# Kernel tuning notes

Hardware: AMD Instinct MI355X
Metric: run time of the kernel (lower is better)

## Reference

```python
import jax, jax.numpy as jnp
import numpy as np

IN_DIM = 128
OUT_DIM = 256
N_ETYPES = 4
N_STEPS = 8
B = 128
N_NODES = 256
E = 393216
CONCAT = IN_DIM + OUT_DIM


def _conv1d(x, w, b):
    # x: [B, C, L], w: [O, I, K] -> valid conv, stride 1
    y = jax.lax.conv_general_dilated(x, w, (1,), 'VALID', dimension_numbers=('NCH', 'OIH', 'NCH'))
    return y + b[None, :, None]


def _maxpool1d(x, k, s):
    return jax.lax.reduce_window(x, -jnp.inf, jax.lax.max, (1, 1, k), (1, 1, s), 'VALID')


def setup_inputs():
    key = jax.random.key(0)
    ks = jax.random.split(key, 16)
    Nn = B * N_NODES
    sc = 0.05
    f32 = jnp.float32
    return {
        'features': jax.random.normal(ks[0], (Nn, IN_DIM), f32),
        'src': jax.random.randint(ks[1], (E,), 0, Nn),
        'dst': jax.random.randint(ks[2], (E,), 0, Nn),
        'etype': jax.random.randint(ks[3], (E,), 0, N_ETYPES),
        'W_msg': jax.random.normal(ks[4], (N_ETYPES, OUT_DIM, OUT_DIM), f32) * sc,
        'b_msg': jnp.zeros((N_ETYPES, OUT_DIM), f32),
        'gru_Wi': jax.random.normal(ks[5], (OUT_DIM, 3 * OUT_DIM), f32) * sc,
        'gru_Wh': jax.random.normal(ks[6], (OUT_DIM, 3 * OUT_DIM), f32) * sc,
        'gru_bi': jnp.zeros((3 * OUT_DIM,), f32),
        'gru_bh': jnp.zeros((3 * OUT_DIM,), f32),
        'conv1_w': jax.random.normal(ks[7], (OUT_DIM, OUT_DIM, 3), f32) * sc,
        'conv1_b': jnp.zeros((OUT_DIM,), f32),
        'conv2_w': jax.random.normal(ks[8], (OUT_DIM, OUT_DIM, 1), f32) * sc,
        'conv2_b': jnp.zeros((OUT_DIM,), f32),
        'convc1_w': jax.random.normal(ks[9], (CONCAT, CONCAT, 3), f32) * sc,
        'convc1_b': jnp.zeros((CONCAT,), f32),
        'convc2_w': jax.random.normal(ks[10], (CONCAT, CONCAT, 1), f32) * sc,
        'convc2_b': jnp.zeros((CONCAT,), f32),
        'wy': jax.random.normal(ks[11], (OUT_DIM, 1), f32) * sc,
        'by': jnp.zeros((1,), f32),
        'wz': jax.random.normal(ks[12], (CONCAT, 1), f32) * sc,
        'bz': jnp.zeros((1,), f32),
        'num_graphs': B,
    }


def reference(features, src, dst, etype, W_msg, b_msg, gru_Wi, gru_Wh, gru_bi, gru_bh,
              conv1_w, conv1_b, conv2_w, conv2_b, convc1_w, convc1_b, convc2_w, convc2_b,
              wy, by, wz, bz, num_graphs):
    Nn = features.shape[0]
    # DGL GatedGraphConv: pad input feats up to out_feats
    h = jnp.pad(features, ((0, 0), (0, OUT_DIM - IN_DIM)))
    for _ in range(N_STEPS):
        # per-etype linear transform of all nodes: [Nn, T, O]
        H_all = jnp.einsum('nd,tdo->nto', h, W_msg) + b_msg[None]
        msg = H_all[src, etype]                              # [E, O]
        a = jax.ops.segment_sum(msg, dst, num_segments=Nn)   # [Nn, O]
        gi = a @ gru_Wi + gru_bi
        gh = h @ gru_Wh + gru_bh
        ir, iz, ig = jnp.split(gi, 3, axis=-1)
        hr, hz, hg = jnp.split(gh, 3, axis=-1)
        r = jax.nn.sigmoid(ir + hr)
        z = jax.nn.sigmoid(iz + hz)
        g = jnp.tanh(ig + r * hg)
        h = (1.0 - z) * g + z * h
    x_i = features.reshape(num_graphs, -1, IN_DIM)
    h_i = h.reshape(num_graphs, -1, OUT_DIM)
    c_i = jnp.concatenate([h_i, x_i], axis=-1)
    Y1 = _maxpool1d(jax.nn.relu(_conv1d(h_i.transpose(0, 2, 1), conv1_w, conv1_b)), 3, 2)
    Y2 = _maxpool1d(jax.nn.relu(_conv1d(Y1, conv2_w, conv2_b)), 2, 2).transpose(0, 2, 1)
    Z1 = _maxpool1d(jax.nn.relu(_conv1d(c_i.transpose(0, 2, 1), convc1_w, convc1_b)), 3, 2)
    Z2 = _maxpool1d(jax.nn.relu(_conv1d(Z1, convc2_w, convc2_b)), 2, 2).transpose(0, 2, 1)
    before_avg = (Y2 @ wy + by) * (Z2 @ wz + bz)   # [B, L, 1]
    avg = before_avg.mean(axis=1)                    # [B, 1]
    return jax.nn.sigmoid(avg).squeeze(-1)           # [B]
```

## Files before the change

### kernel.cpp

```cpp
#include <hip/hip_runtime.h>

#define DEV static __device__ __forceinline__

typedef float f32x4 __attribute__((ext_vector_type(4)));
typedef __bf16 bf16x8 __attribute__((ext_vector_type(8)));
typedef unsigned int u32x4 __attribute__((ext_vector_type(4)));
typedef unsigned int u32x2 __attribute__((ext_vector_type(2)));

#define NNODE 32768
#define NEDGE 393216

DEV unsigned short f2bf(float f) {
    unsigned int u = __builtin_bit_cast(unsigned int, f);
    u += 0x7FFFu + ((u >> 16) & 1u);
    return (unsigned short)(u >> 16);
}
DEV float bf2f(unsigned int b) {
    unsigned int u = b << 16;
    return __builtin_bit_cast(float, u);
}
DEV unsigned int pk2(float a, float b) {
    return (unsigned int)f2bf(a) | ((unsigned int)f2bf(b) << 16);
}
DEV float sigf(float x) { return 1.f / (1.f + __expf(-x)); }

DEV void gld16(const void* g, void* l) {
    __builtin_amdgcn_global_load_lds(
        (const __attribute__((address_space(1))) void*)(g),
        (__attribute__((address_space(3))) void*)(l),
        16, 0, 0);
}


__global__ __launch_bounds__(256) void init_k(
    const float* __restrict__ feat,
    unsigned short* __restrict__ hb0, unsigned short* __restrict__ hb1,
    unsigned short* __restrict__ fb)
{
    int idx = blockIdx.x * 256 + threadIdx.x;
    int r = idx >> 8, c = idx & 255;
    float f = 0.f;
    if (r < NNODE && c < 128) f = feat[(size_t)r * 128 + c];
    unsigned short v = f2bf(f);
    hb0[(size_t)r * 256 + c] = v;
    hb1[(size_t)r * 256 + c] = v;
    if (c < 128) fb[(size_t)r * 128 + c] = v;
}

__global__ __launch_bounds__(256) void prep_wmsg_k(
    const float* __restrict__ Wm, unsigned short* __restrict__ WT)
{
    int idx = blockIdx.x * 256 + threadIdx.x;
    int j = idx >> 8, d = idx & 255;
    int t = j >> 8, o = j & 255;
    WT[idx] = f2bf(Wm[t * 65536 + d * 256 + o]);
}

__global__ __launch_bounds__(256) void prep_gru_k(
    const float* __restrict__ Wi, const float* __restrict__ Wh,
    unsigned short* __restrict__ B2T)
{
    int idx = blockIdx.x * 256 + threadIdx.x;
    int j = idx >> 9, k = idx & 511;
    int band = j >> 6, g = (j >> 4) & 3, ch = (band << 4) + (j & 15);
    float v = 0.f;
    if (g == 0) v = (k < 256) ? Wi[k * 768 + ch] : Wh[(k - 256) * 768 + ch];
    else if (g == 1) v = (k < 256) ? Wi[k * 768 + 256 + ch] : Wh[(k - 256) * 768 + 256 + ch];
    else if (g == 2) { if (k < 256) v = Wi[k * 768 + 512 + ch]; }
    else { if (k >= 256) v = Wh[(k - 256) * 768 + 512 + ch]; }
    B2T[idx] = f2bf(v);
}

__global__ __launch_bounds__(256) void prep_bias2_k(
    const float* __restrict__ bi, const float* __restrict__ bh,
    float* __restrict__ b2)
{
    int j = blockIdx.x * 256 + threadIdx.x;
    int band = j >> 6, g = (j >> 4) & 3, ch = (band << 4) + (j & 15);
    float v;
    if (g == 0) v = bi[ch] + bh[ch];
    else if (g == 1) v = bi[256 + ch] + bh[256 + ch];
    else if (g == 2) v = bi[512 + ch];
    else v = bh[512 + ch];
    b2[j] = v;
}

__global__ __launch_bounds__(256) void prep_conv_k(
    const float* __restrict__ c1w, const float* __restrict__ c2w,
    const float* __restrict__ cc1w, const float* __restrict__ cc2w,
    unsigned short* __restrict__ BTY, unsigned short* __restrict__ BT2,
    unsigned short* __restrict__ BTZ, unsigned short* __restrict__ BTc2)
{
    int idx = blockIdx.x * 256 + threadIdx.x;
    if (idx < 196608) {
        int o = idx / 768, kk = idx - o * 768, k = kk >> 8, c = kk & 255;
        BTY[idx] = f2bf(c1w[o * 768 + c * 3 + k]);
    } else if (idx < 262144) {
        int r = idx - 196608, o = r >> 8, c = r & 255;
        BT2[r] = f2bf(c2w[o * 256 + c]);
    } else if (idx < 704512) {
        int jx = idx - 262144, o = jx / 1152, kk = jx - o * 1152;
        float v;
        if (kk < 768) { int k = kk >> 8, c = kk & 255; v = cc1w[o * 1152 + c * 3 + k]; }
        else { int r = kk - 768, kf = r >> 7, cf = r & 127; v = cc1w[o * 1152 + (256 + cf) * 3 + kf]; }
        BTZ[jx] = f2bf(v);
    } else {
        int r = idx - 704512, o = r / 384, c = r - o * 384;
        BTc2[r] = f2bf(cc2w[o * 384 + c]);
    }
}


__global__ __launch_bounds__(256) void count_k(
    const int* __restrict__ dst, int* __restrict__ cnt)
{
    int e = blockIdx.x * 256 + threadIdx.x;
    atomicAdd(&cnt[dst[e]], 1);
}

__global__ __launch_bounds__(1024) void scan1_k(
    const int* __restrict__ cnt, int* __restrict__ rp, int* __restrict__ bsum)
{
    __shared__ int buf[1024];
    int b = blockIdx.x, tid = threadIdx.x;
    int n = (b << 10) + tid;
    int v = cnt[n];
    buf[tid] = v;
    __syncthreads();
    for (int off = 1; off < 1024; off <<= 1) {
        int x = (tid >= off) ? buf[tid - off] : 0;
        __syncthreads();
        buf[tid] += x;
        __syncthreads();
    }
    rp[n] = buf[tid] - v;
    if (tid == 1023) bsum[b] = buf[1023];
}

__global__ __launch_bounds__(64) void scan2_k(
    const int* __restrict__ bsum, int* __restrict__ boff, int* __restrict__ rp)
{
    int lane = threadIdx.x;
    int v = (lane < 32) ? bsum[lane] : 0;
    int s = v;
    #pragma unroll
    for (int off = 1; off < 32; off <<= 1) {
        int x = __shfl_up(s, off, 64);
        if (lane >= off) s += x;
    }
    if (lane < 32) boff[lane] = s - v;
    if (lane == 31) rp[NNODE] = s;
}

__global__ __launch_bounds__(1024) void scan3_k(
    int* __restrict__ rp, const int* __restrict__ boff)
{
    int b = blockIdx.x, tid = threadIdx.x;
    rp[(b << 10) + tid] += boff[b];
}

__global__ __launch_bounds__(256) void fill_k(
    const int* __restrict__ src, const int* __restrict__ dst,
    const int* __restrict__ et, const int* __restrict__ rp,
    int* __restrict__ pos, int* __restrict__ edat)
{
    int e = blockIdx.x * 256 + threadIdx.x;
    int d = dst[e];
    int p = atomicAdd(&pos[d], 1);
    edat[rp[d] + p] = src[e] | (et[e] << 20);
}


__global__ __launch_bounds__(256) void agg2_k(
    const int* __restrict__ rp, const int* __restrict__ edat,
    const unsigned short* __restrict__ Hmsg, unsigned short* __restrict__ Aonly)
{
    int wave = threadIdx.x >> 6, lane = threadIdx.x & 63;
    int n = (blockIdx.x << 2) + wave;
    int e0 = rp[n], e1 = rp[n + 1];
    float a0 = 0.f, a1 = 0.f, a2 = 0.f, a3 = 0.f;
    const unsigned short* hc = Hmsg + (lane << 2);
    int e = e0;
    for (; e + 8 <= e1; e += 8) {
        u32x2 v[8];
        #pragma unroll
        for (int q = 0; q < 8; q++) {
            int d = edat[e + q];
            v[q] = *(const u32x2*)(hc + ((size_t)(d & 0xFFFFF) << 10) + ((d >> 20) << 8));
        }
        #pragma unroll
        for (int q = 0; q < 8; q++) {
            a0 += bf2f(v[q].x & 0xFFFFu); a1 += bf2f(v[q].x >> 16);
            a2 += bf2f(v[q].y & 0xFFFFu); a3 += bf2f(v[q].y >> 16);
        }
    }
    for (; e < e1; e++) {
        int d = edat[e];
        u32x2 v = *(const u32x2*)(hc + ((size_t)(d & 0xFFFFF) << 10) + ((d >> 20) << 8));
        a0 += bf2f(v.x & 0xFFFFu); a1 += bf2f(v.x >> 16);
        a2 += bf2f(v.y & 0xFFFFu); a3 += bf2f(v.y >> 16);
    }
    u32x2 p; p.x = pk2(a0, a1); p.y = pk2(a2, a3);
    *(u32x2*)(Aonly + (size_t)n * 256 + (lane << 2)) = p;
}

#define STAGE_COORDS                                            \
    int srow[4], scb[4], soff[4];                               \
    _Pragma("unroll")                                           \
    for (int p = 0; p < 4; p++) {                               \
        int c = wave + p * 4;                                   \
        int half = c >> 3, cc = c & 7;                          \
        srow[p] = cc * 16 + (lane >> 2);                        \
        scb[p] = (((lane & 3) ^ ((lane >> 3) & 3)) + half * 4) * 8; \
        soff[p] = half * 4096 + cc * 512;                       \
    }

#define MFMA64(AS, BS)                                                        \
    _Pragma("unroll")                                                         \
    for (int h = 0; h < 2; h++) {                                             \
        bf16x8 af[4], bfr[4];                                                 \
        _Pragma("unroll")                                                     \
        for (int i = 0; i < 4; i++)                                           \
            af[i] = *(const bf16x8*)(&(AS)[h * 4096 + (qm + i * 16 + fm) * 32 + fksw * 8]); \
        _Pragma("unroll")                                                     \
        for (int i = 0; i < 4; i++)                                           \
            bfr[i] = *(const bf16x8*)(&(BS)[h * 4096 + (qn + i * 16 + fm) * 32 + fksw * 8]); \
        _Pragma("unroll")                                                     \
        for (int i = 0; i < 4; i++)                                           \
            _Pragma("unroll")                                                 \
            for (int j = 0; j < 4; j++)                                       \
                acc[i][j] = __builtin_amdgcn_mfma_f32_16x16x32_bf16(bfr[j], af[i], acc[i][j], 0, 0, 0); \
    }

__global__ __launch_bounds__(256) void gemm_bt(
    const unsigned short* __restrict__ A, int lda,
    const unsigned short* __restrict__ Bt,
    unsigned short* __restrict__ Cb, int ldcb,
    const float* __restrict__ bias,
    int N, int K, int swz, int relu)
{
    __shared__ __align__(16) unsigned short As0[128 * 64];
    __shared__ __align__(16) unsigned short As1[128 * 64];
    __shared__ __align__(16) unsigned short Bs0[128 * 64];
    __shared__ __align__(16) unsigned short Bs1[128 * 64];
    const int tid = threadIdx.x;
    int id = blockIdx.x;
    if (swz) { int per = gridDim.x >> 3; id = (id & 7) * per + (id >> 3); }
    const int nb = N >> 7;
    const int bm = id / nb, bn = id - bm * nb;
    const int wave = tid >> 6, lane = tid & 63;
    const unsigned short* Ag = A + (size_t)(bm * 128) * lda;
    const unsigned short* Bg = Bt + (size_t)(bn * 128) * K;
    const int qm = (wave & 1) << 6, qn = (wave >> 1) << 6;
    const int fm = lane & 15, fkv = lane >> 4;
    const int fksw = fkv ^ ((fm >> 1) & 3);
    STAGE_COORDS

    auto stageA = [&](int kb, unsigned short* dst) {
        #pragma unroll
        for (int p = 0; p < 4; p++)
            gld16(Ag + (size_t)srow[p] * lda + kb + scb[p], dst + soff[p]);
    };
    auto stageB = [&](int kb, unsigned short* dst) {
        #pragma unroll
        for (int p = 0; p < 4; p++)
            gld16(Bg + (size_t)srow[p] * K + kb + scb[p], dst + soff[p]);
    };

    f32x4 acc[4][4] = {};

    stageA(0, As0); stageB(0, Bs0);
    __syncthreads();
    unsigned short *Ac = As0, *An = As1, *Bc = Bs0, *Bn = Bs1;
    for (int kb = 0; kb < K; kb += 64) {
        if (kb + 64 < K) { stageA(kb + 64, An); stageB(kb + 64, Bn); }
        MFMA64(Ac, Bc)
        __syncthreads();
        { auto t = Ac; Ac = An; An = t; }
        { auto t = Bc; Bc = Bn; Bn = t; }
    }

    const int m0 = bm * 128 + qm + fm;
    const int n0 = bn * 128 + qn + (fkv << 2);
    #pragma unroll
    for (int i = 0; i < 4; i++) {
        int row = m0 + i * 16;
        #pragma unroll
        for (int j = 0; j < 4; j++) {
            int col = n0 + j * 16;
            float v0 = acc[i][j][0], v1 = acc[i][j][1],
                  v2 = acc[i][j][2], v3 = acc[i][j][3];
            if (bias) {
                float4 bv = *(const float4*)(bias + col);
                v0 += bv.x; v1 += bv.y; v2 += bv.z; v3 += bv.w;
            }
            if (relu) {
                v0 = fmaxf(v0, 0.f); v1 = fmaxf(v1, 0.f);
                v2 = fmaxf(v2, 0.f); v3 = fmaxf(v3, 0.f);
            }
            u32x2 p; p.x = pk2(v0, v1); p.y = pk2(v2, v3);
            *(u32x2*)(Cb + (size_t)row * ldcb + col) = p;
        }
    }
}

__global__ __launch_bounds__(256) void gemm_conv(
    const unsigned short* __restrict__ Ah,
    const unsigned short* __restrict__ Af,
    const unsigned short* __restrict__ Bt,
    unsigned short* __restrict__ Cb, int ldcb,
    const float* __restrict__ bias,
    int N, int K)
{
    __shared__ __align__(16) unsigned short As0[128 * 64];
    __shared__ __align__(16) unsigned short As1[128 * 64];
    __shared__ __align__(16) unsigned short Bs0[128 * 64];
    __shared__ __align__(16) unsigned short Bs1[128 * 64];
    const int tid = threadIdx.x;
    int id = blockIdx.x;
    { int per = gridDim.x >> 3; id = (id & 7) * per + (id >> 3); }
    const int nb = N >> 7;
    const int bm = id / nb, bn = id - bm * nb;
    const int wave = tid >> 6, lane = tid & 63;
    const unsigned short* Bg = Bt + (size_t)(bn * 128) * K;
    const int qm = (wave & 1) << 6, qn = (wave >> 1) << 6;
    const int fm = lane & 15, fkv = lane >> 4;
    const int fksw = fkv ^ ((fm >> 1) & 3);
    STAGE_COORDS

    auto stageA = [&](int kb, unsigned short* dst) {
        const unsigned short* base; int ldA, col, shift;
        if (kb < 768) { base = Ah; ldA = 256; shift = kb >> 8; col = kb & 255; }
        else { int r = kb - 768; base = Af; ldA = 128; shift = r >> 7; col = r & 127; }
        const unsigned short* Ag = base + (size_t)(bm * 128 + shift) * ldA + col;
        #pragma unroll
        for (int p = 0; p < 4; p++)
            gld16(Ag + (size_t)srow[p] * ldA + scb[p], dst + soff[p]);
    };
    auto stageB = [&](int kb, unsigned short* dst) {
        #pragma unroll
        for (int p = 0; p < 4; p++)
            gld16(Bg + (size_t)srow[p] * K + kb + scb[p], dst + soff[p]);
    };

    f32x4 acc[4][4] = {};

    stageA(0, As0); stageB(0, Bs0);
    __syncthreads();
    unsigned short *Ac = As0, *An = As1, *Bc = Bs0, *Bn = Bs1;
    for (int kb = 0; kb < K; kb += 64) {
        if (kb + 64 < K) { stageA(kb + 64, An); stageB(kb + 64, Bn); }
        MFMA64(Ac, Bc)
        __syncthreads();
        { auto t = Ac; Ac = An; An = t; }
        { auto t = Bc; Bc = Bn; Bn = t; }
    }

    const int m0 = bm * 128 + qm + fm;
    const int n0 = bn * 128 + qn + (fkv << 2);
    #pragma unroll
    for (int i = 0; i < 4; i++) {
        int row = m0 + i * 16;
        #pragma unroll
        for (int j = 0; j < 4; j++) {
            int col = n0 + j * 16;
            float4 bv = *(const float4*)(bias + col);
            float v0 = fmaxf(acc[i][j][0] + bv.x, 0.f);
            float v1 = fmaxf(acc[i][j][1] + bv.y, 0.f);
            float v2 = fmaxf(acc[i][j][2] + bv.z, 0.f);
            float v3 = fmaxf(acc[i][j][3] + bv.w, 0.f);
            u32x2 p; p.x = pk2(v0, v1); p.y = pk2(v2, v3);
            *(u32x2*)(Cb + (size_t)row * ldcb + col) = p;
        }
    }
}

__global__ __launch_bounds__(256) void gemm_gru(
    const unsigned short* __restrict__ Aonly,
    const unsigned short* __restrict__ hbc,
    const unsigned short* __restrict__ Bt,
    const float* __restrict__ b2p,
    unsigned short* __restrict__ hbn)
{
    __shared__ __align__(16) unsigned short As0[128 * 64];
    __shared__ __align__(16) unsigned short As1[128 * 64];
    __shared__ __align__(16) unsigned short Bs0[128 * 64];
    __shared__ __align__(16) unsigned short Bs1[128 * 64];
    const int tid = threadIdx.x;
    int id = blockIdx.x;
    { int per = gridDim.x >> 3; id = (id & 7) * per + (id >> 3); }
    const int bm = id >> 3;
    const int bn = id & 7;
    const int wave = tid >> 6, lane = tid & 63;
    const unsigned short* Bg = Bt + (size_t)(bn * 128) * 512;
    const int qm = (wave & 1) << 6, qn = (wave >> 1) << 6;
    const int fm = lane & 15, fkv = lane >> 4;
    const int fksw = fkv ^ ((fm >> 1) & 3);
    STAGE_COORDS

    auto stageA = [&](int kb, unsigned short* dst) {
        const unsigned short* base = (kb < 256) ? Aonly : hbc;
        const unsigned short* Ag = base + (size_t)(bm * 128) * 256 + (kb & 255);
        #pragma unroll
        for (int p = 0; p < 4; p++)
            gld16(Ag + (size_t)srow[p] * 256 + scb[p], dst + soff[p]);
    };
    auto stageB = [&](int kb, unsigned short* dst) {
        #pragma unroll
        for (int p = 0; p < 4; p++)
            gld16(Bg + (size_t)srow[p] * 512 + kb + scb[p], dst + soff[p]);
    };

    f32x4 acc[4][4] = {};

    stageA(0, As0); stageB(0, Bs0);
    __syncthreads();
    unsigned short *Ac = As0, *An = As1, *Bc = Bs0, *Bn = Bs1;
    #pragma unroll
    for (int kb = 0; kb < 512; kb += 64) {
        if (kb < 448) { stageA(kb + 64, An); stageB(kb + 64, Bn); }
        MFMA64(Ac, Bc)
        __syncthreads();
        { auto t = Ac; Ac = An; An = t; }
        { auto t = Bc; Bc = Bn; Bn = t; }
    }

    const int band = (bn << 1) + (qn >> 6);
    const int chb = (band << 4) + (fkv << 2);
    const float4 brv = *(const float4*)(b2p + (band << 6) + 0  + (fkv << 2));
    const float4 bzv = *(const float4*)(b2p + (band << 6) + 16 + (fkv << 2));
    const float4 bgv = *(const float4*)(b2p + (band << 6) + 32 + (fkv << 2));
    const float4 bhv = *(const float4*)(b2p + (band << 6) + 48 + (fkv << 2));
    const float br_[4] = {brv.x, brv.y, brv.z, brv.w};
    const float bz_[4] = {bzv.x, bzv.y, bzv.z, bzv.w};
    const float bg_[4] = {bgv.x, bgv.y, bgv.z, bgv.w};
    const float bh_[4] = {bhv.x, bhv.y, bhv.z, bhv.w};
    const int m0 = bm * 128 + qm + fm;
    #pragma unroll
    for (int i = 0; i < 4; i++) {
        int row = m0 + i * 16;
        u32x2 hv = *(const u32x2*)(hbc + (size_t)row * 256 + chb);
        float hp[4] = {bf2f(hv.x & 0xFFFFu), bf2f(hv.x >> 16),
                       bf2f(hv.y & 0xFFFFu), bf2f(hv.y >> 16)};
        float hn[4];
        #pragma unroll
        for (int r = 0; r < 4; r++) {
            float rg = sigf(acc[i][0][r] + br_[r]);
            float zz = sigf(acc[i][1][r] + bz_[r]);
            float pre = acc[i][2][r] + bg_[r] + rg * (acc[i][3][r] + bh_[r]);
            pre = fminf(fmaxf(pre, -15.f), 15.f);
            float t = __expf(2.f * pre);
            float gq = (t - 1.f) / (t + 1.f);
            hn[r] = (1.f - zz) * gq + zz * hp[r];
        }
        u32x2 p; p.x = pk2(hn[0], hn[1]); p.y = pk2(hn[2], hn[3]);
        *(u32x2*)(hbn + (size_t)row * 256 + chb) = p;
    }
}

__global__ __launch_bounds__(256) void pool_k(
    const unsigned short* __restrict__ in, int ldin, int Lb_in, int L_out,
    int win, int C,
    unsigned short* __restrict__ ob, int ldo)
{
    int idx = blockIdx.x * 256 + threadIdx.x;
    int c = idx % C;
    int row = idx / C;
    int b = row / L_out, lp = row - b * L_out;
    const unsigned short* p = in + (size_t)(b * Lb_in + 2 * lp) * ldin + c;
    float m = bf2f(p[0]);
    for (int d = 1; d < win; d++) m = fmaxf(m, bf2f(p[(size_t)d * ldin]));
    ob[(size_t)row * ldo + c] = f2bf(m);
}

__global__ __launch_bounds__(64) void final_k(
    const unsigned short* __restrict__ CY, const unsigned short* __restrict__ CZ,
    const float* __restrict__ wy, const float* __restrict__ by,
    const float* __restrict__ wz, const float* __restrict__ bz,
    float* __restrict__ out)
{
    int b = blockIdx.x, lane = threadIdx.x;
    float val = 0.f;
    if (lane < 63) {
        const unsigned short* y0 = CY + (size_t)(b * 126 + 2 * lane) * 256;
        const unsigned short* y1 = y0 + 256;
        float y = 0.f;
        for (int o = 0; o < 256; o++)
            y += fmaxf(bf2f(y0[o]), bf2f(y1[o])) * wy[o];
        y += by[0];
        const unsigned short* z0 = CZ + (size_t)(b * 126 + 2 * lane) * 384;
        const unsigned short* z1 = z0 + 384;
        float z = 0.f;
        for (int o = 0; o < 384; o++)
            z += fmaxf(bf2f(z0[o]), bf2f(z1[o])) * wz[o];
        z += bz[0];
        val = y * z;
    }
    for (int off = 32; off > 0; off >>= 1) val += __shfl_down(val, off, 64);
    if (lane == 0) out[b] = sigf(val * (1.f / 63.f));
}


extern "C" void kernel_launch(void* const* d_in, const int* in_sizes, int n_in,
                              void* d_out, int out_size, void* d_ws, size_t ws_size,
                              hipStream_t stream)
{
    const float* feat = (const float*)d_in[0];
    const int* src = (const int*)d_in[1];
    const int* dst = (const int*)d_in[2];
    const int* et  = (const int*)d_in[3];
    const float* Wm  = (const float*)d_in[4];
    const float* bm  = (const float*)d_in[5];
    const float* Wi  = (const float*)d_in[6];
    const float* Wh  = (const float*)d_in[7];
    const float* bi  = (const float*)d_in[8];
    const float* bh  = (const float*)d_in[9];
    const float* c1w = (const float*)d_in[10];
    const float* c1b = (const float*)d_in[11];
    const float* c2w = (const float*)d_in[12];
    const float* c2b = (const float*)d_in[13];
    const float* cc1w = (const float*)d_in[14];
    const float* cc1b = (const float*)d_in[15];
    const float* cc2w = (const float*)d_in[16];
    const float* cc2b = (const float*)d_in[17];
    const float* wy = (const float*)d_in[18];
    const float* by = (const float*)d_in[19];
    const float* wz = (const float*)d_in[20];
    const float* bz = (const float*)d_in[21];
    float* out = (float*)d_out;

    char* w = (char*)d_ws;
    size_t off = 0;
    auto alloc = [&](size_t bytes) -> char* {
        char* p = w + off; off += (bytes + 255) & ~(size_t)255; return p;
    };
    unsigned short* hb0 = (unsigned short*)alloc((size_t)(NNODE + 8) * 256 * 2);
    unsigned short* hb1 = (unsigned short*)alloc((size_t)(NNODE + 8) * 256 * 2);
    unsigned short* fb  = (unsigned short*)alloc((size_t)(NNODE + 8) * 128 * 2);
    unsigned short* Aonly = (unsigned short*)alloc((size_t)NNODE * 256 * 2);
    char* R = alloc((size_t)NNODE * 1024 * 2);
    unsigned short* Hmsg = (unsigned short*)R;
    unsigned short* CbY  = (unsigned short*)R;
    unsigned short* CbZ  = (unsigned short*)(R + (size_t)NNODE * 256 * 2);
    unsigned short* P    = (unsigned short*)alloc((size_t)16128 * 384 * 2);
    unsigned short* Cb2Y = (unsigned short*)alloc((size_t)16128 * 256 * 2);
    unsigned short* Cb2Z = (unsigned short*)alloc((size_t)16128 * 384 * 2);
    unsigned short* WT   = (unsigned short*)alloc(1024 * 256 * 2);
    unsigned short* B2T  = (unsigned short*)alloc(1024 * 512 * 2);
    float* b2            = (float*)alloc(1024 * 4);
    unsigned short* BTY  = (unsigned short*)alloc(256 * 768 * 2);
    unsigned short* BT2  = (unsigned short*)alloc(256 * 256 * 2);
    unsigned short* BTZ  = (unsigned short*)alloc(384 * 1152 * 2);
    unsigned short* BTc2 = (unsigned short*)alloc(384 * 384 * 2);
    int* rp     = (int*)alloc((NNODE + 1) * 4);
    int* pos    = (int*)alloc(NNODE * 4);
    int* cnt    = (int*)alloc(NNODE * 4);
    int* bsum   = (int*)alloc(32 * 4);
    int* boff   = (int*)alloc(32 * 4);
    int* edat   = (int*)alloc(NEDGE * 4);

    hipLaunchKernelGGL(init_k, dim3(NNODE + 8), dim3(256), 0, stream, feat, hb0, hb1, fb);
    hipLaunchKernelGGL(prep_wmsg_k, dim3(1024), dim3(256), 0, stream, Wm, WT);
    hipLaunchKernelGGL(prep_gru_k, dim3(2048), dim3(256), 0, stream, Wi, Wh, B2T);
    hipLaunchKernelGGL(prep_bias2_k, dim3(4), dim3(256), 0, stream, bi, bh, b2);
    hipLaunchKernelGGL(prep_conv_k, dim3(3328), dim3(256), 0, stream,
                       c1w, c2w, cc1w, cc2w, BTY, BT2, BTZ, BTc2);
    hipMemsetAsync(pos, 0, NNODE * 4, stream);
    hipMemsetAsync(cnt, 0, NNODE * 4, stream);
    hipLaunchKernelGGL(count_k, dim3(NEDGE / 256), dim3(256), 0, stream, dst, cnt);
    hipLaunchKernelGGL(scan1_k, dim3(32), dim3(1024), 0, stream, cnt, rp, bsum);
    hipLaunchKernelGGL(scan2_k, dim3(1), dim3(64), 0, stream, bsum, boff, rp);
    hipLaunchKernelGGL(scan3_k, dim3(32), dim3(1024), 0, stream, rp, boff);
    hipLaunchKernelGGL(fill_k, dim3(NEDGE / 256), dim3(256), 0, stream, src, dst, et, rp, pos, edat);

    unsigned short* hbuf[2] = {hb0, hb1};
    for (int step = 0; step < 8; step++) {
        unsigned short* cur = hbuf[step & 1];
        unsigned short* nxt = hbuf[(step + 1) & 1];
        hipLaunchKernelGGL(gemm_bt, dim3(2048), dim3(256), 0, stream,
            cur, 256, WT, Hmsg, 1024, bm, 1024, 256, 1, 0);
        hipLaunchKernelGGL(agg2_k, dim3(NNODE / 4), dim3(256), 0, stream, rp, edat, Hmsg, Aonly);
        hipLaunchKernelGGL(gemm_gru, dim3(2048), dim3(256), 0, stream,
            Aonly, cur, B2T, b2, nxt);
    }

    hipLaunchKernelGGL(gemm_conv, dim3(512), dim3(256), 0, stream,
        hb0, (const unsigned short*)nullptr, BTY, CbY, 256, c1b, 256, 768);
    hipLaunchKernelGGL(pool_k, dim3(16128), dim3(256), 0, stream,
        CbY, 256, 256, 126, 3, 256, P, 256);
    hipLaunchKernelGGL(gemm_bt, dim3(252), dim3(256), 0, stream,
        P, 256, BT2, Cb2Y, 256, c2b, 256, 256, 0, 1);

    hipLaunchKernelGGL(gemm_conv, dim3(768), dim3(256), 0, stream,
        hb0, fb, BTZ, CbZ, 384, cc1b, 384, 1152);
    hipLaunchKernelGGL(pool_k, dim3(24192), dim3(256), 0, stream,
        CbZ, 384, 256, 126, 3, 384, P, 384);
    hipLaunchKernelGGL(gemm_bt, dim3(378), dim3(256), 0, stream,
        P, 384, BTc2, Cb2Z, 384, cc2b, 384, 384, 0, 1);

    hipLaunchKernelGGL(final_k, dim3(128), dim3(64), 0, stream,
        Cb2Y, Cb2Z, wy, by, wz, bz, out);
}
```

Measured before the change: 1.323 ms.

## Fuse all eight GGNN steps into one persistent kernel with grid barriers

Replaces the 24 per-step launches (message GEMM, edge aggregation, GRU GEMM) with a single persistent kernel sized to occupancy that loops over steps and phases and separates them with a software atomic grid barrier. The aim is to remove launch overhead and inter-kernel gaps. In exchange, each phase now runs on a fixed grid of at most 512 blocks doing strided tile loops, which may lower parallelism and latency hiding. The spin barrier also depends on every block being co-resident on the device.

```diff
diff --git a/kernel.cpp b/kernel.cpp
--- a/kernel.cpp
+++ b/kernel.cpp
@@ -170,40 +170,6 @@
     edat[rp[d] + p] = src[e] | (et[e] << 20);
 }
 
-
-__global__ __launch_bounds__(256) void agg2_k(
-    const int* __restrict__ rp, const int* __restrict__ edat,
-    const unsigned short* __restrict__ Hmsg, unsigned short* __restrict__ Aonly)
-{
-    int wave = threadIdx.x >> 6, lane = threadIdx.x & 63;
-    int n = (blockIdx.x << 2) + wave;
-    int e0 = rp[n], e1 = rp[n + 1];
-    float a0 = 0.f, a1 = 0.f, a2 = 0.f, a3 = 0.f;
-    const unsigned short* hc = Hmsg + (lane << 2);
-    int e = e0;
-    for (; e + 8 <= e1; e += 8) {
-        u32x2 v[8];
-        #pragma unroll
-        for (int q = 0; q < 8; q++) {
-            int d = edat[e + q];
-            v[q] = *(const u32x2*)(hc + ((size_t)(d & 0xFFFFF) << 10) + ((d >> 20) << 8));
-        }
-        #pragma unroll
-        for (int q = 0; q < 8; q++) {
-            a0 += bf2f(v[q].x & 0xFFFFu); a1 += bf2f(v[q].x >> 16);
-            a2 += bf2f(v[q].y & 0xFFFFu); a3 += bf2f(v[q].y >> 16);
-        }
-    }
-    for (; e < e1; e++) {
-        int d = edat[e];
-        u32x2 v = *(const u32x2*)(hc + ((size_t)(d & 0xFFFFF) << 10) + ((d >> 20) << 8));
-        a0 += bf2f(v.x & 0xFFFFu); a1 += bf2f(v.x >> 16);
-        a2 += bf2f(v.y & 0xFFFFu); a3 += bf2f(v.y >> 16);
-    }
-    u32x2 p; p.x = pk2(a0, a1); p.y = pk2(a2, a3);
-    *(u32x2*)(Aonly + (size_t)n * 256 + (lane << 2)) = p;
-}
-
 #define STAGE_COORDS                                            \
     int srow[4], scb[4], soff[4];                               \
     _Pragma("unroll")                                           \
@@ -231,6 +197,190 @@
             for (int j = 0; j < 4; j++)                                       \
                 acc[i][j] = __builtin_amdgcn_mfma_f32_16x16x32_bf16(bfr[j], af[i], acc[i][j], 0, 0, 0); \
     }
+
+__global__ __launch_bounds__(256, 2) void steps_k(
+    const int* __restrict__ rp, const int* __restrict__ edat,
+    unsigned short* __restrict__ hb0, unsigned short* __restrict__ hb1,
+    const unsigned short* __restrict__ WT, const float* __restrict__ bmsg,
+    const unsigned short* __restrict__ B2T, const float* __restrict__ b2p,
+    unsigned short* __restrict__ Hmsg, unsigned short* __restrict__ Aonly,
+    int* __restrict__ bar_cnt, int* __restrict__ bar_gen, int G)
+{
+    __shared__ __align__(16) unsigned short As0[128 * 64];
+    __shared__ __align__(16) unsigned short As1[128 * 64];
+    __shared__ __align__(16) unsigned short Bs0[128 * 64];
+    __shared__ __align__(16) unsigned short Bs1[128 * 64];
+    const int tid = threadIdx.x;
+    const int wave = tid >> 6, lane = tid & 63;
+    const int qm = (wave & 1) << 6, qn = (wave >> 1) << 6;
+    const int fm = lane & 15, fkv = lane >> 4;
+    const int fksw = fkv ^ ((fm >> 1) & 3);
+    STAGE_COORDS
+    int lgen = 0;
+
+    auto gridbar = [&]() {
+        __syncthreads();
+        if (tid == 0) {
+            __threadfence();
+            lgen++;
+            int old = atomicAdd(bar_cnt, 1);
+            if (old == G * lgen - 1) atomicAdd(bar_gen, 1);
+            while (atomicAdd(bar_gen, 0) < lgen) __builtin_amdgcn_s_sleep(8);
+            __threadfence();
+        }
+        __syncthreads();
+    };
+
+    for (int step = 0; step < 8; step++) {
+        const unsigned short* cur = (step & 1) ? hb1 : hb0;
+        unsigned short* nxt = (step & 1) ? hb0 : hb1;
+
+        for (int s = blockIdx.x; s < 512; s += G) {
+            const int xcd = s & 7, lx = s >> 3;
+            for (int r = 0; r < 4; r++) {
+                const int tl = lx + (r << 6);
+                const int bm = (xcd << 5) + (tl >> 3), bn = tl & 7;
+                const unsigned short* Ag = cur + (((size_t)bm) << 7) * 256;
+                const unsigned short* Bg = WT + (((size_t)bn) << 7) * 256;
+                auto stA = [&](int kb, unsigned short* d) {
+                    #pragma unroll
+                    for (int p = 0; p < 4; p++)
+                        gld16(Ag + (size_t)srow[p] * 256 + kb + scb[p], d + soff[p]);
+                };
+                auto stB = [&](int kb, unsigned short* d) {
+                    #pragma unroll
+                    for (int p = 0; p < 4; p++)
+                        gld16(Bg + (size_t)srow[p] * 256 + kb + scb[p], d + soff[p]);
+                };
+                f32x4 acc[4][4] = {};
+                stA(0, As0); stB(0, Bs0);
+                __syncthreads();
+                unsigned short *Ac = As0, *An = As1, *Bc = Bs0, *Bn2 = Bs1;
+                #pragma unroll
+                for (int kb = 0; kb < 256; kb += 64) {
+                    if (kb < 192) { stA(kb + 64, An); stB(kb + 64, Bn2); }
+                    MFMA64(Ac, Bc)
+                    __syncthreads();
+                    { auto t = Ac; Ac = An; An = t; }
+                    { auto t = Bc; Bc = Bn2; Bn2 = t; }
+                }
+                const int m0 = (bm << 7) + qm + fm;
+                const int n0 = (bn << 7) + qn + (fkv << 2);
+                #pragma unroll
+                for (int i = 0; i < 4; i++) {
+                    int row = m0 + i * 16;
+                    #pragma unroll
+                    for (int j = 0; j < 4; j++) {
+                        int col = n0 + j * 16;
+                        float4 bv = *(const float4*)(bmsg + col);
+                        u32x2 p;
+                        p.x = pk2(acc[i][j][0] + bv.x, acc[i][j][1] + bv.y);
+                        p.y = pk2(acc[i][j][2] + bv.z, acc[i][j][3] + bv.w);
+                        *(u32x2*)(Hmsg + (size_t)row * 1024 + col) = p;
+                    }
+                }
+            }
+        }
+        gridbar();
+
+        for (int s = blockIdx.x; s < 512; s += G) {
+            for (int i = 0; i < 16; i++) {
+                int n = (s << 6) + (wave << 4) + i;
+                int e0 = rp[n], e1 = rp[n + 1];
+                float a0 = 0.f, a1 = 0.f, a2 = 0.f, a3 = 0.f;
+                const unsigned short* hc = Hmsg + (lane << 2);
+                int e = e0;
+                for (; e + 8 <= e1; e += 8) {
+                    u32x2 v[8];
+                    #pragma unroll
+                    for (int q = 0; q < 8; q++) {
+                        int d = edat[e + q];
+                        v[q] = *(const u32x2*)(hc + ((size_t)(d & 0xFFFFF) << 10) + ((d >> 20) << 8));
+                    }
+                    #pragma unroll
+                    for (int q = 0; q < 8; q++) {
+                        a0 += bf2f(v[q].x & 0xFFFFu); a1 += bf2f(v[q].x >> 16);
+                        a2 += bf2f(v[q].y & 0xFFFFu); a3 += bf2f(v[q].y >> 16);
+                    }
+                }
+                for (; e < e1; e++) {
+                    int d = edat[e];
+                    u32x2 v = *(const u32x2*)(hc + ((size_t)(d & 0xFFFFF) << 10) + ((d >> 20) << 8));
+                    a0 += bf2f(v.x & 0xFFFFu); a1 += bf2f(v.x >> 16);
+                    a2 += bf2f(v.y & 0xFFFFu); a3 += bf2f(v.y >> 16);
+                }
+                u32x2 p; p.x = pk2(a0, a1); p.y = pk2(a2, a3);
+                *(u32x2*)(Aonly + (size_t)n * 256 + (lane << 2)) = p;
+            }
+        }
+        gridbar();
+
+        for (int s = blockIdx.x; s < 512; s += G) {
+            const int xcd = s & 7, lx = s >> 3;
+            for (int r = 0; r < 4; r++) {
+                const int tl = lx + (r << 6);
+                const int bm = (xcd << 5) + (tl >> 3), bn = tl & 7;
+                const unsigned short* Bg = B2T + (((size_t)bn) << 7) * 512;
+                auto stA = [&](int kb, unsigned short* d) {
+                    const unsigned short* base = (kb < 256) ? Aonly : cur;
+                    const unsigned short* Ag = base + (((size_t)bm) << 7) * 256 + (kb & 255);
+                    #pragma unroll
+                    for (int p = 0; p < 4; p++)
+                        gld16(Ag + (size_t)srow[p] * 256 + scb[p], d + soff[p]);
+                };
+                auto stB = [&](int kb, unsigned short* d) {
+                    #pragma unroll
+                    for (int p = 0; p < 4; p++)
+                        gld16(Bg + (size_t)srow[p] * 512 + kb + scb[p], d + soff[p]);
+                };
+                f32x4 acc[4][4] = {};
+                stA(0, As0); stB(0, Bs0);
+                __syncthreads();
+                unsigned short *Ac = As0, *An = As1, *Bc = Bs0, *Bn2 = Bs1;
+                #pragma unroll
+                for (int kb = 0; kb < 512; kb += 64) {
+                    if (kb < 448) { stA(kb + 64, An); stB(kb + 64, Bn2); }
+                    MFMA64(Ac, Bc)
+                    __syncthreads();
+                    { auto t = Ac; Ac = An; An = t; }
+                    { auto t = Bc; Bc = Bn2; Bn2 = t; }
+                }
+                const int band = (bn << 1) + (qn >> 6);
+                const int chb = (band << 4) + (fkv << 2);
+                const float4 brv = *(const float4*)(b2p + (band << 6) + 0  + (fkv << 2));
+                const float4 bzv = *(const float4*)(b2p + (band << 6) + 16 + (fkv << 2));
+                const float4 bgv = *(const float4*)(b2p + (band << 6) + 32 + (fkv << 2));
+                const float4 bhv = *(const float4*)(b2p + (band << 6) + 48 + (fkv << 2));
+                const float br_[4] = {brv.x, brv.y, brv.z, brv.w};
+                const float bz_[4] = {bzv.x, bzv.y, bzv.z, bzv.w};
+                const float bg_[4] = {bgv.x, bgv.y, bgv.z, bgv.w};
+                const float bh_[4] = {bhv.x, bhv.y, bhv.z, bhv.w};
+                const int m0 = (bm << 7) + qm + fm;
+                #pragma unroll
+                for (int i = 0; i < 4; i++) {
+                    int row = m0 + i * 16;
+                    u32x2 hv = *(const u32x2*)(cur + (size_t)row * 256 + chb);
+                    float hp[4] = {bf2f(hv.x & 0xFFFFu), bf2f(hv.x >> 16),
+                                   bf2f(hv.y & 0xFFFFu), bf2f(hv.y >> 16)};
+                    float hn[4];
+                    #pragma unroll
+                    for (int rr = 0; rr < 4; rr++) {
+                        float rg = sigf(acc[i][0][rr] + br_[rr]);
+                        float zz = sigf(acc[i][1][rr] + bz_[rr]);
+                        float pre = acc[i][2][rr] + bg_[rr] + rg * (acc[i][3][rr] + bh_[rr]);
+                        pre = fminf(fmaxf(pre, -15.f), 15.f);
+                        float t = __expf(2.f * pre);
+                        float gq = (t - 1.f) / (t + 1.f);
+                        hn[rr] = (1.f - zz) * gq + zz * hp[rr];
+                    }
+                    u32x2 p; p.x = pk2(hn[0], hn[1]); p.y = pk2(hn[2], hn[3]);
+                    *(u32x2*)(nxt + (size_t)row * 256 + chb) = p;
+                }
+            }
+        }
+        if (step < 7) gridbar();
+    }
+}
 
 __global__ __launch_bounds__(256) void gemm_bt(
     const unsigned short* __restrict__ A, int lda,
@@ -372,89 +522,6 @@
             u32x2 p; p.x = pk2(v0, v1); p.y = pk2(v2, v3);
             *(u32x2*)(Cb + (size_t)row * ldcb + col) = p;
         }
-    }
-}
-
-__global__ __launch_bounds__(256) void gemm_gru(
-    const unsigned short* __restrict__ Aonly,
-    const unsigned short* __restrict__ hbc,
-    const unsigned short* __restrict__ Bt,
-    const float* __restrict__ b2p,
-    unsigned short* __restrict__ hbn)
-{
-    __shared__ __align__(16) unsigned short As0[128 * 64];
-    __shared__ __align__(16) unsigned short As1[128 * 64];
-    __shared__ __align__(16) unsigned short Bs0[128 * 64];
-    __shared__ __align__(16) unsigned short Bs1[128 * 64];
-    const int tid = threadIdx.x;
-    int id = blockIdx.x;
-    { int per = gridDim.x >> 3; id = (id & 7) * per + (id >> 3); }
-    const int bm = id >> 3;
-    const int bn = id & 7;
-    const int wave = tid >> 6, lane = tid & 63;
-    const unsigned short* Bg = Bt + (size_t)(bn * 128) * 512;
-    const int qm = (wave & 1) << 6, qn = (wave >> 1) << 6;
-    const int fm = lane & 15, fkv = lane >> 4;
-    const int fksw = fkv ^ ((fm >> 1) & 3);
-    STAGE_COORDS
-
-    auto stageA = [&](int kb, unsigned short* dst) {
-        const unsigned short* base = (kb < 256) ? Aonly : hbc;
-        const unsigned short* Ag = base + (size_t)(bm * 128) * 256 + (kb & 255);
-        #pragma unroll
-        for (int p = 0; p < 4; p++)
-            gld16(Ag + (size_t)srow[p] * 256 + scb[p], dst + soff[p]);
-    };
-    auto stageB = [&](int kb, unsigned short* dst) {
-        #pragma unroll
-        for (int p = 0; p < 4; p++)
-            gld16(Bg + (size_t)srow[p] * 512 + kb + scb[p], dst + soff[p]);
-    };
-
-    f32x4 acc[4][4] = {};
-
-    stageA(0, As0); stageB(0, Bs0);
-    __syncthreads();
-    unsigned short *Ac = As0, *An = As1, *Bc = Bs0, *Bn = Bs1;
-    #pragma unroll
-    for (int kb = 0; kb < 512; kb += 64) {
-        if (kb < 448) { stageA(kb + 64, An); stageB(kb + 64, Bn); }
-        MFMA64(Ac, Bc)
-        __syncthreads();
-        { auto t = Ac; Ac = An; An = t; }
-        { auto t = Bc; Bc = Bn; Bn = t; }
-    }
-
-    const int band = (bn << 1) + (qn >> 6);
-    const int chb = (band << 4) + (fkv << 2);
-    const float4 brv = *(const float4*)(b2p + (band << 6) + 0  + (fkv << 2));
-    const float4 bzv = *(const float4*)(b2p + (band << 6) + 16 + (fkv << 2));
-    const float4 bgv = *(const float4*)(b2p + (band << 6) + 32 + (fkv << 2));
-    const float4 bhv = *(const float4*)(b2p + (band << 6) + 48 + (fkv << 2));
-    const float br_[4] = {brv.x, brv.y, brv.z, brv.w};
-    const float bz_[4] = {bzv.x, bzv.y, bzv.z, bzv.w};
-    const float bg_[4] = {bgv.x, bgv.y, bgv.z, bgv.w};
-    const float bh_[4] = {bhv.x, bhv.y, bhv.z, bhv.w};
-    const int m0 = bm * 128 + qm + fm;
-    #pragma unroll
-    for (int i = 0; i < 4; i++) {
-        int row = m0 + i * 16;
-        u32x2 hv = *(const u32x2*)(hbc + (size_t)row * 256 + chb);
-        float hp[4] = {bf2f(hv.x & 0xFFFFu), bf2f(hv.x >> 16),
-                       bf2f(hv.y & 0xFFFFu), bf2f(hv.y >> 16)};
-        float hn[4];
-        #pragma unroll
-        for (int r = 0; r < 4; r++) {
-            float rg = sigf(acc[i][0][r] + br_[r]);
-            float zz = sigf(acc[i][1][r] + bz_[r]);
-            float pre = acc[i][2][r] + bg_[r] + rg * (acc[i][3][r] + bh_[r]);
-            pre = fminf(fmaxf(pre, -15.f), 15.f);
-            float t = __expf(2.f * pre);
-            float gq = (t - 1.f) / (t + 1.f);
-            hn[r] = (1.f - zz) * gq + zz * hp[r];
-        }
-        u32x2 p; p.x = pk2(hn[0], hn[1]); p.y = pk2(hn[2], hn[3]);
-        *(u32x2*)(hbn + (size_t)row * 256 + chb) = p;
     }
 }
 
@@ -558,6 +625,18 @@
     int* bsum   = (int*)alloc(32 * 4);
     int* boff   = (int*)alloc(32 * 4);
     int* edat   = (int*)alloc(NEDGE * 4);
+    int* bar    = (int*)alloc(2 * 4);
+
+    static int ngrid = 0;
+    if (ngrid == 0) {
+        int perCU = 0;
+        hipOccupancyMaxActiveBlocksPerMultiprocessor(&perCU, steps_k, 256, 0);
+        hipDeviceProp_t prop;
+        hipGetDeviceProperties(&prop, 0);
+        int cap = perCU * prop.multiProcessorCount;
+        ngrid = cap < 512 ? cap : 512;
+        if (ngrid < 1) ngrid = 1;
+    }
 
     hipLaunchKernelGGL(init_k, dim3(NNODE + 8), dim3(256), 0, stream, feat, hb0, hb1, fb);
     hipLaunchKernelGGL(prep_wmsg_k, dim3(1024), dim3(256), 0, stream, Wm, WT);
@@ -567,22 +646,16 @@
                        c1w, c2w, cc1w, cc2w, BTY, BT2, BTZ, BTc2);
     hipMemsetAsync(pos, 0, NNODE * 4, stream);
     hipMemsetAsync(cnt, 0, NNODE * 4, stream);
+    hipMemsetAsync(bar, 0, 2 * 4, stream);
     hipLaunchKernelGGL(count_k, dim3(NEDGE / 256), dim3(256), 0, stream, dst, cnt);
     hipLaunchKernelGGL(scan1_k, dim3(32), dim3(1024), 0, stream, cnt, rp, bsum);
     hipLaunchKernelGGL(scan2_k, dim3(1), dim3(64), 0, stream, bsum, boff, rp);
     hipLaunchKernelGGL(scan3_k, dim3(32), dim3(1024), 0, stream, rp, boff);
     hipLaunchKernelGGL(fill_k, dim3(NEDGE / 256), dim3(256), 0, stream, src, dst, et, rp, pos, edat);
 
-    unsigned short* hbuf[2] = {hb0, hb1};
-    for (int step = 0; step < 8; step++) {
-        unsigned short* cur = hbuf[step & 1];
-        unsigned short* nxt = hbuf[(step + 1) & 1];
-        hipLaunchKernelGGL(gemm_bt, dim3(2048), dim3(256), 0, stream,
-            cur, 256, WT, Hmsg, 1024, bm, 1024, 256, 1, 0);
-        hipLaunchKernelGGL(agg2_k, dim3(NNODE / 4), dim3(256), 0, stream, rp, edat, Hmsg, Aonly);
-        hipLaunchKernelGGL(gemm_gru, dim3(2048), dim3(256), 0, stream,
-            Aonly, cur, B2T, b2, nxt);
-    }
+    hipLaunchKernelGGL(steps_k, dim3(ngrid), dim3(256), 0, stream,
+        rp, edat, hb0, hb1, WT, bm, B2T, b2, Hmsg, Aonly,
+        bar + 0, bar + 1, ngrid);
 
     hipLaunchKernelGGL(gemm_conv, dim3(512), dim3(256), 0, stream,
         hb0, (const unsigned short*)nullptr, BTY, CbY, 256, c1b, 256, 768);
```

Measured after the change: 2.390 ms. +80.6%, slower.
